# Performance work log

Measured on AMD Instinct MI355X. Metric: run time of the kernel, lower is better.

## Reference

```python
import jax, jax.numpy as jnp
import numpy as np

HEAD_NUM = 16
KEY_DIM = 64
EMBED = 1024
KV_OUT = HEAD_NUM * KEY_DIM  # 1024


def setup_inputs() -> dict:
    key = jax.random.key(0)
    ks = jax.random.split(key, 11)
    B, L, E = 2, 2048, EMBED
    scale = 0.02
    return {
        "query": jax.random.normal(ks[0], (B, L, E), jnp.float32),
        "key": jax.random.normal(ks[1], (B, L, E), jnp.float32),
        "value": jax.random.normal(ks[2], (B, L, E), jnp.float32),
        "W_Query": jax.random.normal(ks[3], (E, KV_OUT), jnp.float32) * scale,
        "W_Key": jax.random.normal(ks[4], (E, KV_OUT), jnp.float32) * scale,
        "W_Value": jax.random.normal(ks[5], (E, KV_OUT), jnp.float32) * scale,
        "W_Output": jax.random.normal(ks[6], (KV_OUT, E), jnp.float32) * scale,
        "B_Query": jnp.zeros((KV_OUT,), jnp.float32),
        "B_Key": jnp.zeros((KV_OUT,), jnp.float32),
        "B_Value": jnp.zeros((KV_OUT,), jnp.float32),
        "B_Output": jnp.zeros((E,), jnp.float32),
    }


def reference(query, key, value, W_Query, W_Key, W_Value, W_Output,
              B_Query, B_Key, B_Value, B_Output):
    B, Lq, E = query.shape
    Lk = key.shape[1]
    H, D = HEAD_NUM, KEY_DIM
    # QKV projections + bias
    q = query @ W_Query + B_Query            # [B, Lq, H*D]
    k = key @ W_Key + B_Key                  # [B, Lk, H*D]
    v = value @ W_Value + B_Value            # [B, Lk, H*D]
    # tf.split(axis=2) per head == reshape to [B, L, H, D]
    q = q.reshape(B, Lq, H, D)
    k = k.reshape(B, Lk, H, D)
    v = v.reshape(B, Lk, H, D)
    # scaled dot-product attention (no mask, dropout=0)
    scores = jnp.einsum("bqhd,bkhd->bhqk", q, k) / (D ** 0.5)
    probs = jax.nn.softmax(scores, axis=-1)
    out = jnp.einsum("bhqk,bkhd->bqhd", probs, v)  # [B, Lq, H, D]
    out = out.reshape(B, Lq, H * D)
    return out @ W_Output + B_Output
```

## Files before the change

kernel.cpp:

```cpp
#include <hip/hip_runtime.h>

using u16 = unsigned short;
using u32 = unsigned int;

typedef __attribute__((ext_vector_type(8))) short bf16x8;
typedef __attribute__((ext_vector_type(4))) float f32x4;
typedef __attribute__((ext_vector_type(4))) u32 u32x4;
typedef __attribute__((ext_vector_type(2))) u32 u32x2;
typedef __attribute__((ext_vector_type(4))) _Float16 f16x4;

#define MFMA_BF16_K32(a, b, c) __builtin_amdgcn_mfma_f32_16x16x32_bf16((a), (b), (c), 0, 0, 0)
#define MFMA_F16_K16(a, b, c) __builtin_amdgcn_mfma_f32_16x16x16f16((a), (b), (c), 0, 0, 0)

#define QSCALE 0.18033688011112042f

extern "C" __device__ float __ocml_native_exp2_f32(float);

__device__ __forceinline__ u16 f2bf(float f) {
  u32 u = __builtin_bit_cast(u32, f);
  return (u16)((u + 0x7fffu + ((u >> 16) & 1u)) >> 16);
}

__device__ __forceinline__ u32 pk_f16(float a, float b) {
  auto v = __builtin_amdgcn_cvt_pkrtz(a, b);
  return __builtin_bit_cast(u32, v);
}

__device__ __forceinline__ void load_lds16(const void* g, void* l) {
  __builtin_amdgcn_global_load_lds((__attribute__((address_space(1))) void*)g,
                                   (__attribute__((address_space(3))) void*)l,
                                   16, 0, 0);
}

__global__ __launch_bounds__(256) void cvt_all_kernel(
    const float* __restrict__ q, const float* __restrict__ k, const float* __restrict__ v,
    u16* __restrict__ oq, u16* __restrict__ ok, u16* __restrict__ ov,
    const float* __restrict__ w0, const float* __restrict__ w1,
    const float* __restrict__ w2, const float* __restrict__ w3,
    u16* __restrict__ d0, u16* __restrict__ d1,
    u16* __restrict__ d2, u16* __restrict__ d3) {
  const int id = blockIdx.x;
  const int tid = threadIdx.x;
  if (id < 6144) {
    const int z = id >> 11, bx = id & 2047;
    const float* s = z == 0 ? q : z == 1 ? k : v;
    u16* d = z == 0 ? oq : z == 1 ? ok : ov;
    int i = (bx * 256 + tid) * 8;
    f32x4 a = *(const f32x4*)(s + i);
    f32x4 b = *(const f32x4*)(s + i + 4);
    u32x4 o;
    o.x = (u32)f2bf(a.x) | ((u32)f2bf(a.y) << 16);
    o.y = (u32)f2bf(a.z) | ((u32)f2bf(a.w) << 16);
    o.z = (u32)f2bf(b.x) | ((u32)f2bf(b.y) << 16);
    o.w = (u32)f2bf(b.z) | ((u32)f2bf(b.w) << 16);
    *(u32x4*)(d + i) = o;
    return;
  }
  __shared__ float t[64][65];
  const int r0 = id - 6144;
  const int z = r0 >> 8, rr0 = r0 & 255;
  const int bx = rr0 & 15, by = rr0 >> 4;
  const float* src = z == 0 ? w0 : z == 1 ? w1 : z == 2 ? w2 : w3;
  u16* dst = z == 0 ? d0 : z == 1 ? d1 : z == 2 ? d2 : d3;
  const float scale = (z == 0) ? QSCALE : 1.0f;
  const int r = tid >> 4, c4 = (tid & 15) * 4;
#pragma unroll
  for (int i = 0; i < 4; ++i) {
    int row = r + i * 16;
    f32x4 vv = *(const f32x4*)(src + (by * 64 + row) * 1024 + bx * 64 + c4);
    t[row][c4 + 0] = vv.x;
    t[row][c4 + 1] = vv.y;
    t[row][c4 + 2] = vv.z;
    t[row][c4 + 3] = vv.w;
  }
  __syncthreads();
  const int rw = tid >> 2, cc = (tid & 3) * 16;
  alignas(16) u16 tmp[16];
#pragma unroll
  for (int j = 0; j < 16; ++j) tmp[j] = f2bf(t[cc + j][rw] * scale);
  u32x4* outp = (u32x4*)(dst + (bx * 64 + rw) * 1024 + by * 64 + cc);
  outp[0] = *(const u32x4*)&tmp[0];
  outp[1] = *(const u32x4*)&tmp[8];
}

__global__ __launch_bounds__(256) void gemm_qkv_kernel(
    const u16* __restrict__ x0, const u16* __restrict__ x1, const u16* __restrict__ x2,
    const u16* __restrict__ w0, const u16* __restrict__ w1, const u16* __restrict__ w2,
    const float* __restrict__ b0, const float* __restrict__ b1, const float* __restrict__ b2,
    u16* __restrict__ c0, u16* __restrict__ c1, u16* __restrict__ vt) {
  __shared__ u16 As[128 * 64];
  __shared__ u16 Bs[128 * 64];
  const int lid = blockIdx.x;
  const int xcd = lid & 7, rr = lid >> 3;
  const int nb = rr & 7, slot = rr >> 3;
  const int g = slot * 8 + xcd;
  const int z = g >> 5, m_idx = g & 31;
  const u16* A = z == 0 ? x0 : z == 1 ? x1 : x2;
  const u16* Bt = z == 0 ? w0 : z == 1 ? w1 : w2;
  const float* bias = z == 0 ? b0 : z == 1 ? b1 : b2;
  const float bscale = z == 0 ? QSCALE : 1.0f;
  const int tid = threadIdx.x;
  const int wave = tid >> 6, lane = tid & 63;
  const int l16 = lane & 15, quad = lane >> 4;
  const int l7 = l16 & 7;
  const int wm = wave >> 1, wn = wave & 1;
  const int m0 = m_idx * 128, n0 = nb * 128;

  f32x4 acc[4][4];
  const f32x4 zf = {0.f, 0.f, 0.f, 0.f};
#pragma unroll
  for (int i = 0; i < 4; ++i)
#pragma unroll
    for (int j = 0; j < 4; ++j) acc[i][j] = zf;

  for (int kb = 0; kb < 1024; kb += 64) {
#pragma unroll
    for (int t = 0; t < 4; ++t) {
      int c = wave * 256 + t * 64 + lane;
      int row = c >> 3, sc8 = (c & 7) ^ (row & 7);
      load_lds16(A + (m0 + row) * 1024 + kb + sc8 * 8, &As[(wave * 256 + t * 64) * 8]);
    }
#pragma unroll
    for (int t = 0; t < 4; ++t) {
      int c = wave * 256 + t * 64 + lane;
      int row = c >> 3, sc8 = (c & 7) ^ (row & 7);
      load_lds16(Bt + (n0 + row) * 1024 + kb + sc8 * 8, &Bs[(wave * 256 + t * 64) * 8]);
    }
    asm volatile("s_waitcnt vmcnt(0)" ::: "memory");
    __syncthreads();
#pragma unroll
    for (int ks = 0; ks < 2; ++ks) {
      const int sch = (ks * 4 + quad) ^ l7;
      bf16x8 af[4], bfv[4];
#pragma unroll
      for (int mt = 0; mt < 4; ++mt)
        af[mt] = *(const bf16x8*)&As[(wm * 64 + mt * 16 + l16) * 64 + sch * 8];
#pragma unroll
      for (int nt = 0; nt < 4; ++nt)
        bfv[nt] = *(const bf16x8*)&Bs[(wn * 64 + nt * 16 + l16) * 64 + sch * 8];
#pragma unroll
      for (int mt = 0; mt < 4; ++mt)
#pragma unroll
        for (int nt = 0; nt < 4; ++nt) acc[mt][nt] = MFMA_BF16_K32(af[mt], bfv[nt], acc[mt][nt]);
    }
    __syncthreads();
  }

  float bv[4];
#pragma unroll
  for (int nt = 0; nt < 4; ++nt) bv[nt] = bias[n0 + wn * 64 + nt * 16 + l16] * bscale;
  if (z != 2) {
    u16* C = z == 0 ? c0 : c1;
#pragma unroll
    for (int mt = 0; mt < 4; ++mt)
#pragma unroll
      for (int nt = 0; nt < 4; ++nt)
#pragma unroll
        for (int r = 0; r < 4; ++r) {
          int row = m0 + wm * 64 + mt * 16 + quad * 4 + r;
          int col = n0 + wn * 64 + nt * 16 + l16;
          C[row * 1024 + col] = f2bf(acc[mt][nt][r] + bv[nt]);
        }
  } else {
#pragma unroll
    for (int mt = 0; mt < 4; ++mt)
#pragma unroll
      for (int nt = 0; nt < 4; ++nt)
#pragma unroll
        for (int r = 0; r < 4; ++r) {
          int row = m0 + wm * 64 + mt * 16 + quad * 4 + r;
          int col = n0 + wn * 64 + nt * 16 + l16;
          int bb = row >> 11, kv = row & 2047;
          _Float16 hv = (_Float16)(acc[mt][nt][r] + bv[nt]);
          vt[(bb * 1024 + col) * 2048 + kv] = __builtin_bit_cast(u16, hv);
        }
  }
}

__global__ __launch_bounds__(256) void gemm_out_kernel(const u16* __restrict__ A,
                                                       const u16* __restrict__ Bt,
                                                       const float* __restrict__ bias,
                                                       float* __restrict__ C) {
  __shared__ u16 As[64 * 64];
  __shared__ u16 Bs[128 * 64];
  const int lid = blockIdx.x;
  const int xcd = lid & 7, rr = lid >> 3;
  const int nb = rr & 7, slot = rr >> 3;
  const int by = slot * 8 + xcd;
  const int tid = threadIdx.x;
  const int wave = tid >> 6, lane = tid & 63;
  const int l16 = lane & 15, quad = lane >> 4;
  const int l7 = l16 & 7;
  const int m0 = by * 64, n0 = nb * 128;

  f32x4 acc[4][2];
  const f32x4 zf = {0.f, 0.f, 0.f, 0.f};
#pragma unroll
  for (int i = 0; i < 4; ++i)
#pragma unroll
    for (int j = 0; j < 2; ++j) acc[i][j] = zf;

  for (int kb = 0; kb < 1024; kb += 64) {
#pragma unroll
    for (int t = 0; t < 2; ++t) {
      int c = wave * 128 + t * 64 + lane;
      int row = c >> 3, sc8 = (c & 7) ^ (row & 7);
      load_lds16(A + (m0 + row) * 1024 + kb + sc8 * 8, &As[(wave * 128 + t * 64) * 8]);
    }
#pragma unroll
    for (int t = 0; t < 4; ++t) {
      int c = wave * 256 + t * 64 + lane;
      int row = c >> 3, sc8 = (c & 7) ^ (row & 7);
      load_lds16(Bt + (n0 + row) * 1024 + kb + sc8 * 8, &Bs[(wave * 256 + t * 64) * 8]);
    }
    asm volatile("s_waitcnt vmcnt(0)" ::: "memory");
    __syncthreads();
#pragma unroll
    for (int ks = 0; ks < 2; ++ks) {
      const int sch = (ks * 4 + quad) ^ l7;
      bf16x8 af[4], bfv[2];
#pragma unroll
      for (int mt = 0; mt < 4; ++mt)
        af[mt] = *(const bf16x8*)&As[(mt * 16 + l16) * 64 + sch * 8];
#pragma unroll
      for (int nt = 0; nt < 2; ++nt)
        bfv[nt] = *(const bf16x8*)&Bs[(wave * 32 + nt * 16 + l16) * 64 + sch * 8];
#pragma unroll
      for (int mt = 0; mt < 4; ++mt)
#pragma unroll
        for (int nt = 0; nt < 2; ++nt) acc[mt][nt] = MFMA_BF16_K32(af[mt], bfv[nt], acc[mt][nt]);
    }
    __syncthreads();
  }

  float bv[2];
#pragma unroll
  for (int nt = 0; nt < 2; ++nt) bv[nt] = bias[n0 + wave * 32 + nt * 16 + l16];
#pragma unroll
  for (int mt = 0; mt < 4; ++mt)
#pragma unroll
    for (int nt = 0; nt < 2; ++nt)
#pragma unroll
      for (int r = 0; r < 4; ++r) {
        int row = m0 + mt * 16 + quad * 4 + r;
        int col = n0 + wave * 32 + nt * 16 + l16;
        C[row * 1024 + col] = acc[mt][nt][r] + bv[nt];
      }
}

__global__ __launch_bounds__(256, 2) void flash_kernel(const u16* __restrict__ Q,
                                                       const u16* __restrict__ K,
                                                       const u16* __restrict__ Vt,
                                                       u16* __restrict__ O) {
  __shared__ u16 k_lds[128 * 64];
  __shared__ u16 vt_lds[64 * 128];
  __shared__ float lred[4][64];
  __shared__ float lfin[64];
  const int tid = threadIdx.x;
  const int wave = tid >> 6, lane = tid & 63;
  const int l16 = lane & 15, quad = lane >> 4;
  const int l7 = l16 & 7;
  const int id = blockIdx.x;
  const int xcd = id & 7, slot = id >> 3;
  const int pair = xcd * 4 + (slot & 3);
  const int qb = slot >> 2;
  const int b = pair >> 4, h = pair & 15;
  const u16* Qh = Q + (b * 2048 + qb * 64) * 1024 + h * 64;
  const u16* Kh = K + b * 2048 * 1024 + h * 64;
  const u16* Vh = Vt + pair * 64 * 2048;

#pragma unroll
  for (int t = 0; t < 2; ++t) {
    int c = (t * 4 + wave) * 64 + lane;
    int row = c >> 3, sc8 = (c & 7) ^ (row & 7);
    load_lds16(Qh + row * 1024 + sc8 * 8, &k_lds[((t * 4 + wave) * 64) * 8]);
  }
  asm volatile("s_waitcnt vmcnt(0)" ::: "memory");
  __syncthreads();
  bf16x8 qf[4][2];
#pragma unroll
  for (int qn = 0; qn < 4; ++qn)
#pragma unroll
    for (int ks = 0; ks < 2; ++ks)
      qf[qn][ks] = *(const bf16x8*)&k_lds[(qn * 16 + l16) * 64 + (((ks * 4 + quad) ^ l7)) * 8];
  __syncthreads();

  f32x4 o_acc[4][4];
  const f32x4 zf = {0.f, 0.f, 0.f, 0.f};
#pragma unroll
  for (int qn = 0; qn < 4; ++qn)
#pragma unroll
    for (int dt = 0; dt < 4; ++dt) o_acc[qn][dt] = zf;
  float lp[4] = {0.f, 0.f, 0.f, 0.f};

  for (int kb = 0; kb < 16; ++kb) {
    const int kv0 = kb * 128;
#pragma unroll
    for (int t = 0; t < 4; ++t) {
      int c = (t * 4 + wave) * 64 + lane;
      int row = c >> 3, sc8 = (c & 7) ^ (row & 7);
      load_lds16(Kh + (kv0 + row) * 1024 + sc8 * 8, &k_lds[((t * 4 + wave) * 64) * 8]);
    }
#pragma unroll
    for (int t = 0; t < 4; ++t) {
      int c = (t * 4 + wave) * 64 + lane;
      int d = c >> 4, sc = (c & 15) ^ (d & 15);
      load_lds16(Vh + d * 2048 + kv0 + sc * 8, &vt_lds[((t * 4 + wave) * 64) * 8]);
    }
    asm volatile("s_waitcnt vmcnt(0)" ::: "memory");
    __syncthreads();

#pragma unroll
    for (int c2 = 0; c2 < 2; ++c2) {
      const int chunk = wave * 2 + c2;
      f32x4 s_acc[4];
#pragma unroll
      for (int qn = 0; qn < 4; ++qn) s_acc[qn] = zf;
#pragma unroll
      for (int ks = 0; ks < 2; ++ks) {
        bf16x8 kf = *(const bf16x8*)&k_lds[(chunk * 16 + l16) * 64 + ((ks * 4 + quad) ^ l7) * 8];
#pragma unroll
        for (int qn = 0; qn < 4; ++qn) s_acc[qn] = MFMA_BF16_K32(kf, qf[qn][ks], s_acc[qn]);
      }
      union { u32 u[2]; f16x4 v; } pkv[4];
#pragma unroll
      for (int qn = 0; qn < 4; ++qn) {
        float e0 = __ocml_native_exp2_f32(s_acc[qn].x);
        float e1 = __ocml_native_exp2_f32(s_acc[qn].y);
        float e2 = __ocml_native_exp2_f32(s_acc[qn].z);
        float e3 = __ocml_native_exp2_f32(s_acc[qn].w);
        lp[qn] += (e0 + e1) + (e2 + e3);
        pkv[qn].u[0] = pk_f16(e0, e1);
        pkv[qn].u[1] = pk_f16(e2, e3);
      }
#pragma unroll
      for (int dt = 0; dt < 4; ++dt) {
        f16x4 vf = *(const f16x4*)&vt_lds[(dt * 16 + l16) * 128 +
                                          (((chunk * 2 + (quad >> 1)) ^ l16) * 8) + (quad & 1) * 4];
#pragma unroll
        for (int qn = 0; qn < 4; ++qn)
          o_acc[qn][dt] = MFMA_F16_K16(pkv[qn].v, vf, o_acc[qn][dt]);
      }
    }
    __syncthreads();
  }

#pragma unroll
  for (int qn = 0; qn < 4; ++qn) {
    lp[qn] += __shfl_xor(lp[qn], 16);
    lp[qn] += __shfl_xor(lp[qn], 32);
  }
  if (quad == 0) {
#pragma unroll
    for (int qn = 0; qn < 4; ++qn) lred[wave][qn * 16 + l16] = lp[qn];
  }
  float* bufA = (float*)k_lds;
  float* bufB = (float*)vt_lds;
  if (wave == 1 || wave == 3) {
    float* buf = (wave == 1) ? bufA : bufB;
#pragma unroll
    for (int qm = 0; qm < 4; ++qm)
#pragma unroll
      for (int dt = 0; dt < 4; ++dt)
        *(f32x4*)&buf[(((qm * 4 + dt) * 4 + quad) * 16 + l16) * 4] = o_acc[qm][dt];
  }
  __syncthreads();
  if (tid < 64) lfin[tid] = lred[0][tid] + lred[1][tid] + lred[2][tid] + lred[3][tid];
  if (wave == 0 || wave == 2) {
    float* buf = (wave == 0) ? bufA : bufB;
#pragma unroll
    for (int qm = 0; qm < 4; ++qm)
#pragma unroll
      for (int dt = 0; dt < 4; ++dt)
        o_acc[qm][dt] += *(const f32x4*)&buf[(((qm * 4 + dt) * 4 + quad) * 16 + l16) * 4];
  }
  __syncthreads();
  if (wave == 2) {
#pragma unroll
    for (int qm = 0; qm < 4; ++qm)
#pragma unroll
      for (int dt = 0; dt < 4; ++dt)
        *(f32x4*)&bufA[(((qm * 4 + dt) * 4 + quad) * 16 + l16) * 4] = o_acc[qm][dt];
  }
  __syncthreads();
  if (wave == 0) {
#pragma unroll
    for (int qm = 0; qm < 4; ++qm)
#pragma unroll
      for (int dt = 0; dt < 4; ++dt)
        o_acc[qm][dt] += *(const f32x4*)&bufA[(((qm * 4 + dt) * 4 + quad) * 16 + l16) * 4];
#pragma unroll
    for (int qm = 0; qm < 4; ++qm)
#pragma unroll
      for (int r = 0; r < 4; ++r) {
        int qrow = qm * 16 + quad * 4 + r;
        float inv = 1.0f / lfin[qrow];
        int row = b * 2048 + qb * 64 + qrow;
#pragma unroll
        for (int dt = 0; dt < 4; ++dt)
          O[row * 1024 + h * 64 + dt * 16 + l16] = f2bf(o_acc[qm][dt][r] * inv);
      }
  }
}

extern "C" void kernel_launch(void* const* d_in, const int* in_sizes, int n_in,
                              void* d_out, int out_size, void* d_ws, size_t ws_size,
                              hipStream_t stream) {
  const float* q = (const float*)d_in[0];
  const float* k = (const float*)d_in[1];
  const float* v = (const float*)d_in[2];
  const float* Wq = (const float*)d_in[3];
  const float* Wk = (const float*)d_in[4];
  const float* Wv = (const float*)d_in[5];
  const float* Wo = (const float*)d_in[6];
  const float* Bq = (const float*)d_in[7];
  const float* Bk = (const float*)d_in[8];
  const float* Bv = (const float*)d_in[9];
  const float* Bo = (const float*)d_in[10];
  float* out = (float*)d_out;

  char* w = (char*)d_ws;
  const size_t MB = 1u << 20;
  u16* xq = (u16*)(w + 0 * MB);
  u16* xk = (u16*)(w + 8 * MB);
  u16* xv = (u16*)(w + 16 * MB);
  u16* wqt = (u16*)(w + 24 * MB);
  u16* wkt = (u16*)(w + 26 * MB);
  u16* wvt = (u16*)(w + 28 * MB);
  u16* wot = (u16*)(w + 30 * MB);
  u16* Qp = (u16*)(w + 32 * MB);
  u16* Kp = (u16*)(w + 40 * MB);
  u16* Vtr = (u16*)(w + 48 * MB);
  u16* At = (u16*)(w + 56 * MB);

  cvt_all_kernel<<<dim3(7168), 256, 0, stream>>>(q, k, v, xq, xk, xv,
                                                 Wq, Wk, Wv, Wo, wqt, wkt, wvt, wot);
  gemm_qkv_kernel<<<dim3(768), 256, 0, stream>>>(xq, xk, xv, wqt, wkt, wvt,
                                                 Bq, Bk, Bv, Qp, Kp, Vtr);
  flash_kernel<<<dim3(1024), 256, 0, stream>>>(Qp, Kp, Vtr, At);
  gemm_out_kernel<<<dim3(512), 256, 0, stream>>>(At, wot, Bo, out);
}
```

Before: 227.4 us.

## Load K and V fragments directly from global memory into registers in flash kernel

```diff
diff --git a/kernel.cpp b/kernel.cpp
--- a/kernel.cpp
+++ b/kernel.cpp
@@ -248,12 +248,12 @@
       }
 }
 
-__global__ __launch_bounds__(256, 2) void flash_kernel(const u16* __restrict__ Q,
-                                                       const u16* __restrict__ K,
-                                                       const u16* __restrict__ Vt,
-                                                       u16* __restrict__ O) {
-  __shared__ u16 k_lds[128 * 64];
-  __shared__ u16 vt_lds[64 * 128];
+__global__ __launch_bounds__(256) void flash_kernel(const u16* __restrict__ Q,
+                                                    const u16* __restrict__ K,
+                                                    const u16* __restrict__ Vt,
+                                                    u16* __restrict__ O) {
+  __shared__ float bufA[4096];
+  __shared__ float bufB[4096];
   __shared__ float lred[4][64];
   __shared__ float lfin[64];
   const int tid = threadIdx.x;
@@ -269,11 +269,12 @@
   const u16* Kh = K + b * 2048 * 1024 + h * 64;
   const u16* Vh = Vt + pair * 64 * 2048;
 
+  u16* qlds = (u16*)bufA;
 #pragma unroll
   for (int t = 0; t < 2; ++t) {
     int c = (t * 4 + wave) * 64 + lane;
     int row = c >> 3, sc8 = (c & 7) ^ (row & 7);
-    load_lds16(Qh + row * 1024 + sc8 * 8, &k_lds[((t * 4 + wave) * 64) * 8]);
+    load_lds16(Qh + row * 1024 + sc8 * 8, &qlds[((t * 4 + wave) * 64) * 8]);
   }
   asm volatile("s_waitcnt vmcnt(0)" ::: "memory");
   __syncthreads();
@@ -282,7 +283,7 @@
   for (int qn = 0; qn < 4; ++qn)
 #pragma unroll
     for (int ks = 0; ks < 2; ++ks)
-      qf[qn][ks] = *(const bf16x8*)&k_lds[(qn * 16 + l16) * 64 + (((ks * 4 + quad) ^ l7)) * 8];
+      qf[qn][ks] = *(const bf16x8*)&qlds[(qn * 16 + l16) * 64 + (((ks * 4 + quad) ^ l7)) * 8];
   __syncthreads();
 
   f32x4 o_acc[4][4];
@@ -295,32 +296,29 @@
 
   for (int kb = 0; kb < 16; ++kb) {
     const int kv0 = kb * 128;
-#pragma unroll
-    for (int t = 0; t < 4; ++t) {
-      int c = (t * 4 + wave) * 64 + lane;
-      int row = c >> 3, sc8 = (c & 7) ^ (row & 7);
-      load_lds16(Kh + (kv0 + row) * 1024 + sc8 * 8, &k_lds[((t * 4 + wave) * 64) * 8]);
-    }
-#pragma unroll
-    for (int t = 0; t < 4; ++t) {
-      int c = (t * 4 + wave) * 64 + lane;
-      int d = c >> 4, sc = (c & 15) ^ (d & 15);
-      load_lds16(Vh + d * 2048 + kv0 + sc * 8, &vt_lds[((t * 4 + wave) * 64) * 8]);
-    }
-    asm volatile("s_waitcnt vmcnt(0)" ::: "memory");
-    __syncthreads();
-
+    u32x4 kf[2][2];
+    u32x2 vf[2][4];
 #pragma unroll
     for (int c2 = 0; c2 < 2; ++c2) {
-      const int chunk = wave * 2 + c2;
+      const int kvrow = kv0 + (wave * 2 + c2) * 16 + l16;
+#pragma unroll
+      for (int ks = 0; ks < 2; ++ks)
+        kf[c2][ks] = *(const u32x4*)(Kh + kvrow * 1024 + ks * 32 + quad * 8);
+      const int kvc = kv0 + (wave * 2 + c2) * 16 + quad * 4;
+#pragma unroll
+      for (int dt = 0; dt < 4; ++dt)
+        vf[c2][dt] = *(const u32x2*)(Vh + (dt * 16 + l16) * 2048 + kvc);
+    }
+#pragma unroll
+    for (int c2 = 0; c2 < 2; ++c2) {
       f32x4 s_acc[4];
 #pragma unroll
       for (int qn = 0; qn < 4; ++qn) s_acc[qn] = zf;
 #pragma unroll
       for (int ks = 0; ks < 2; ++ks) {
-        bf16x8 kf = *(const bf16x8*)&k_lds[(chunk * 16 + l16) * 64 + ((ks * 4 + quad) ^ l7) * 8];
-#pragma unroll
-        for (int qn = 0; qn < 4; ++qn) s_acc[qn] = MFMA_BF16_K32(kf, qf[qn][ks], s_acc[qn]);
+        bf16x8 kfr = __builtin_bit_cast(bf16x8, kf[c2][ks]);
+#pragma unroll
+        for (int qn = 0; qn < 4; ++qn) s_acc[qn] = MFMA_BF16_K32(kfr, qf[qn][ks], s_acc[qn]);
       }
       union { u32 u[2]; f16x4 v; } pkv[4];
 #pragma unroll
@@ -335,14 +333,12 @@
       }
 #pragma unroll
       for (int dt = 0; dt < 4; ++dt) {
-        f16x4 vf = *(const f16x4*)&vt_lds[(dt * 16 + l16) * 128 +
-                                          (((chunk * 2 + (quad >> 1)) ^ l16) * 8) + (quad & 1) * 4];
+        f16x4 vfr = __builtin_bit_cast(f16x4, vf[c2][dt]);
 #pragma unroll
         for (int qn = 0; qn < 4; ++qn)
-          o_acc[qn][dt] = MFMA_F16_K16(pkv[qn].v, vf, o_acc[qn][dt]);
+          o_acc[qn][dt] = MFMA_F16_K16(pkv[qn].v, vfr, o_acc[qn][dt]);
       }
     }
-    __syncthreads();
   }
 
 #pragma unroll
@@ -354,8 +350,6 @@
 #pragma unroll
     for (int qn = 0; qn < 4; ++qn) lred[wave][qn * 16 + l16] = lp[qn];
   }
-  float* bufA = (float*)k_lds;
-  float* bufB = (float*)vt_lds;
   if (wave == 1 || wave == 3) {
     float* buf = (wave == 1) ? bufA : bufB;
 #pragma unroll
```

New measurement: 265.7 us. 16.8% more time.
